# Kernel tuning notes

Hardware: AMD Instinct MI355X
Metric: run time of the kernel (lower is better)

## Reference

```python
import jax, jax.numpy as jnp
import numpy as np

B, T, D, H, O = 128, 2048, 128, 1024, 32
LAST = 20          # last_n_outputs
ALPHA = 0.9        # leak rate
SPARSITY = 0.8


def _make_w_r(rng):
    # Faithful to torch __init__: randn, /max, sparsify, /spectral radius
    w_r = rng.standard_normal((H, H))
    w_r = w_r / np.max(w_r)
    w_r = np.where(rng.random(w_r.shape) < SPARSITY, 0.0, w_r)
    max_abs_eig = np.max(np.abs(np.linalg.eigvals(w_r)))
    return (w_r / max_abs_eig).astype(np.float32)


def setup_inputs() -> dict:
    key = jax.random.key(0)
    k_x, k_in, k_w, k_b = jax.random.split(key, 4)
    rng = np.random.default_rng(0)
    x = jax.random.normal(k_x, (B, T, D), dtype=jnp.float32)
    w_in = jax.random.normal(k_in, (D, H), dtype=jnp.float32) * 0.2
    w_r = jnp.asarray(_make_w_r(rng))
    W = jax.random.normal(k_w, (H * LAST, O), dtype=jnp.float32) * 0.02
    b = jax.random.normal(k_b, (O,), dtype=jnp.float32) * 0.02
    return {"x": x, "w_in": w_in, "w_r": w_r, "W": W, "b": b}


def reference(x, w_in, w_r, W, b):
    # Precompute the non-recurrent term in one batched GEMM: [B,T,H]
    xw = jnp.einsum('btd,dh->bth', x, w_in)

    # t == 0: h0 = 0, and original code sets h = h_hat (no leaky mix)
    h = jnp.tanh(xw[:, 0])  # [B, H]

    def step(h, xt):
        h_hat = jnp.tanh(xt + h @ w_r)
        return (1.0 - ALPHA) * h + ALPHA * h_hat, None

    # steps 1 .. T-LAST-1 : no outputs collected
    xw_mid = jnp.swapaxes(xw[:, 1:T - LAST], 0, 1)   # [T-LAST-1, B, H]
    h, _ = jax.lax.scan(step, h, xw_mid)

    def step_out(h, xt):
        h_hat = jnp.tanh(xt + h @ w_r)
        h_new = (1.0 - ALPHA) * h + ALPHA * h_hat
        return h_new, h_new

    # last LAST steps: collect hidden states
    xw_tail = jnp.swapaxes(xw[:, T - LAST:], 0, 1)   # [LAST, B, H]
    _, hs = jax.lax.scan(step_out, h, xw_tail)       # [LAST, B, H]

    # concat in time order along feature dim -> [B, LAST*H]
    out_cat = jnp.transpose(hs, (1, 0, 2)).reshape(B, LAST * H)
    return out_cat @ W + b
```

## Files before the change

### kernel.cpp

```cpp
#include <hip/hip_runtime.h>
#include <stdint.h>
#include <stddef.h>

#define B_    128
#define T_    2048
#define D_    128
#define H_    1024
#define O_    32
#define LAST_ 20

#define NB_   8
#define NC_   16
#define RING_ 4

typedef __bf16 bf16x8 __attribute__((ext_vector_type(8)));
typedef __bf16 bf16x4 __attribute__((ext_vector_type(4)));
typedef float  f32x4  __attribute__((ext_vector_type(4)));

union Pack8  { unsigned long long u;    bf16x4 v; };
union Pack16 { unsigned long long u[2]; bf16x8 v; };

__device__ __forceinline__ float tanh_fast(float s) {
    float a = fminf(fmaxf(s, -12.0f), 12.0f);
    float e = __expf(2.0f * a);
    return (e - 1.0f) / (e + 1.0f);
}

__global__ __launch_bounds__(256, 1) void esn_persist(
    const float* __restrict__ x, const float* __restrict__ w_in,
    const float* __restrict__ w_r, __bf16* __restrict__ h_ex,
    float* __restrict__ hs)
{
    __shared__ bf16x8 ls[2][16][128];

    const int wg  = (int)blockIdx.x;
    const int bb  = wg & (NB_ - 1);
    const int cb  = wg >> 3;
    const int tid = (int)threadIdx.x;
    const int wv  = tid >> 6;
    const int ln  = tid & 63;
    const int nn  = ln & 15;
    const int q   = ln >> 4;
    const int b0  = bb * 16;
    const int n0  = cb * 64 + wv * 16;

    bf16x8 win[4];
    #pragma unroll
    for (int c = 0; c < 4; ++c) {
        bf16x8 f;
        #pragma unroll
        for (int j = 0; j < 8; ++j)
            f[j] = (__bf16)w_in[(size_t)(c * 32 + q * 8 + j) * H_ + (n0 + nn)];
        win[c] = f;
    }
    bf16x8 wr[32];
    #pragma unroll
    for (int kc = 0; kc < 32; ++kc) {
        bf16x8 f;
        #pragma unroll
        for (int j = 0; j < 8; ++j)
            f[j] = (__bf16)w_r[(size_t)(kc * 32 + q * 8 + j) * H_ + (n0 + nn)];
        wr[kc] = f;
    }

    const unsigned long long tdead =
        __builtin_amdgcn_s_memrealtime() + 300000000ull;

    const float* xrow = x + (size_t)(b0 + nn) * T_ * D_ + q * 8;
    const size_t hrow = (size_t)(b0 + nn) * H_;

    f32x4 xn[8];
    bf16x8 xf[4];
    {
        #pragma unroll
        for (int c = 0; c < 4; ++c) {
            xn[2 * c]     = *(const f32x4*)(xrow + c * 32);
            xn[2 * c + 1] = *(const f32x4*)(xrow + c * 32 + 4);
        }
        #pragma unroll
        for (int c = 0; c < 4; ++c) {
            bf16x8 f;
            #pragma unroll
            for (int j = 0; j < 4; ++j) {
                f[j]     = (__bf16)xn[2 * c][j];
                f[j + 4] = (__bf16)xn[2 * c + 1][j];
            }
            xf[c] = f;
        }
    }

    float hm0 = 0.f, hm1 = 0.f, hm2 = 0.f, hm3 = 0.f;

    for (int t = 0; t < T_; ++t) {
        {
            const int tn = (t + 1 < T_) ? t + 1 : T_ - 1;
            const float* xp = xrow + (size_t)tn * D_;
            #pragma unroll
            for (int c = 0; c < 4; ++c) {
                xn[2 * c]     = *(const f32x4*)(xp + c * 32);
                xn[2 * c + 1] = *(const f32x4*)(xp + c * 32 + 4);
            }
        }

        f32x4 acc0 = {0.f, 0.f, 0.f, 0.f};
        f32x4 acc1 = {0.f, 0.f, 0.f, 0.f};
        f32x4 acc2 = {0.f, 0.f, 0.f, 0.f};
        f32x4 acc3 = {0.f, 0.f, 0.f, 0.f};

        #pragma unroll
        for (int c = 0; c < 4; ++c)
            acc0 = __builtin_amdgcn_mfma_f32_16x16x32_bf16(win[c], xf[c], acc0, 0, 0, 0);

        if (t > 0) {
            const unsigned long long want =
                (unsigned long long)((((t - 1) >> 2) & 1) ^ 1);
            const int sb = (t - 1) & 1;
            const __bf16* hbase = h_ex
                + (size_t)((t - 1) & (RING_ - 1)) * (B_ * H_) + (size_t)b0 * H_;
            Pack16 pk[8];
            int spins = 0;
            for (;;) {
                #pragma unroll
                for (int i = 0; i < 8; ++i) {
                    const int p = wv * 512 + i * 64 + ln;
                    const unsigned long long* gp = (const unsigned long long*)
                        (hbase + (size_t)(p >> 7) * H_ + (p & 127) * 8);
                    pk[i].u[0] = __hip_atomic_load(gp, __ATOMIC_RELAXED,
                                                   __HIP_MEMORY_SCOPE_AGENT);
                    pk[i].u[1] = __hip_atomic_load(gp + 1, __ATOMIC_RELAXED,
                                                   __HIP_MEMORY_SCOPE_AGENT);
                }
                unsigned ok = 1u;
                #pragma unroll
                for (int i = 0; i < 8; ++i) {
                    ok &= (unsigned)((pk[i].u[0] & 1ull) == want);
                    ok &= (unsigned)((pk[i].u[1] & 1ull) == want);
                }
                if (__all(ok != 0u)) break;
                __builtin_amdgcn_s_sleep(1);
                if (((++spins) & 63) == 0 &&
                    __builtin_amdgcn_s_memrealtime() > tdead) break;
            }

            #pragma unroll
            for (int i = 0; i < 8; ++i) {
                const int p = wv * 512 + i * 64 + ln;
                const int r = p >> 7, ch = p & 127;
                ls[sb][r][ch ^ (r & 7)] = pk[i].v;
            }

            __syncthreads();

            #pragma unroll
            for (int kc = 0; kc < 32; ++kc) {
                bf16x8 a = ls[sb][nn][(kc * 4 + q) ^ (nn & 7)];
                if      ((kc & 3) == 0) acc0 = __builtin_amdgcn_mfma_f32_16x16x32_bf16(wr[kc], a, acc0, 0, 0, 0);
                else if ((kc & 3) == 1) acc1 = __builtin_amdgcn_mfma_f32_16x16x32_bf16(wr[kc], a, acc1, 0, 0, 0);
                else if ((kc & 3) == 2) acc2 = __builtin_amdgcn_mfma_f32_16x16x32_bf16(wr[kc], a, acc2, 0, 0, 0);
                else                    acc3 = __builtin_amdgcn_mfma_f32_16x16x32_bf16(wr[kc], a, acc3, 0, 0, 0);
            }
        }

        const f32x4 acc = (acc0 + acc1) + (acc2 + acc3);
        const float th0 = tanh_fast(acc[0]);
        const float th1 = tanh_fast(acc[1]);
        const float th2 = tanh_fast(acc[2]);
        const float th3 = tanh_fast(acc[3]);
        if (t == 0) {
            hm0 = th0; hm1 = th1; hm2 = th2; hm3 = th3;
        } else {
            hm0 = 0.1f * hm0 + 0.9f * th0;
            hm1 = 0.1f * hm1 + 0.9f * th1;
            hm2 = 0.1f * hm2 + 0.9f * th2;
            hm3 = 0.1f * hm3 + 0.9f * th3;
        }

        {
            Pack8 p;
            p.v = (bf16x4){(__bf16)hm0, (__bf16)hm1, (__bf16)hm2, (__bf16)hm3};
            p.u = (p.u & ~1ull) | (unsigned long long)(((t >> 2) & 1) ^ 1);
            unsigned long long* op = (unsigned long long*)
                (h_ex + (size_t)(t & (RING_ - 1)) * (B_ * H_) + hrow + n0 + q * 4);
            __hip_atomic_store(op, p.u, __ATOMIC_RELAXED,
                               __HIP_MEMORY_SCOPE_AGENT);
        }

        if (t >= T_ - LAST_) {
            f32x4* sp = (f32x4*)(hs + (size_t)(t - (T_ - LAST_)) * (B_ * H_)
                                    + hrow + n0 + q * 4);
            *sp = (f32x4){hm0, hm1, hm2, hm3};
        }
        #pragma unroll
        for (int c = 0; c < 4; ++c) {
            bf16x8 f;
            #pragma unroll
            for (int j = 0; j < 4; ++j) {
                f[j]     = (__bf16)xn[2 * c][j];
                f[j + 4] = (__bf16)xn[2 * c + 1][j];
            }
            xf[c] = f;
        }
    }
}

__global__ __launch_bounds__(256) void esn_out(
    const float* __restrict__ hs, const float* __restrict__ Wm,
    const float* __restrict__ bias, float* __restrict__ out)
{
    const int b   = (int)blockIdx.x;
    const int tid = (int)threadIdx.x;
    float acc[O_];
    #pragma unroll
    for (int o = 0; o < O_; ++o) acc[o] = 0.f;

    for (int k = tid; k < LAST_ * H_; k += 256) {
        const float hv = hs[(size_t)(k >> 10) * (B_ * H_) + (size_t)b * H_ + (k & (H_ - 1))];
        const f32x4* wp = (const f32x4*)(Wm + (size_t)k * O_);
        #pragma unroll
        for (int v = 0; v < 8; ++v) {
            f32x4 w4 = wp[v];
            acc[4 * v + 0] = fmaf(hv, w4[0], acc[4 * v + 0]);
            acc[4 * v + 1] = fmaf(hv, w4[1], acc[4 * v + 1]);
            acc[4 * v + 2] = fmaf(hv, w4[2], acc[4 * v + 2]);
            acc[4 * v + 3] = fmaf(hv, w4[3], acc[4 * v + 3]);
        }
    }

    __shared__ float red[256][O_ + 1];
    #pragma unroll
    for (int o = 0; o < O_; ++o) red[tid][o] = acc[o];
    __syncthreads();
    if (tid < O_) {
        float s = bias[tid];
        for (int i = 0; i < 256; ++i) s += red[i][tid];
        out[(size_t)b * O_ + tid] = s;
    }
}

extern "C" void kernel_launch(void* const* d_in, const int* in_sizes, int n_in,
                              void* d_out, int out_size, void* d_ws, size_t ws_size,
                              hipStream_t stream)
{
    const float* x    = (const float*)d_in[0];
    const float* w_in = (const float*)d_in[1];
    const float* w_r  = (const float*)d_in[2];
    const float* Wm   = (const float*)d_in[3];
    const float* bias = (const float*)d_in[4];
    float* out        = (float*)d_out;

    const size_t flag_bytes = 4096;
    const size_t hex_bytes  = (size_t)RING_ * B_ * H_ * sizeof(__bf16);
    const size_t hs_bytes   = (size_t)LAST_ * B_ * H_ * sizeof(float);
    if (ws_size < flag_bytes + hex_bytes + hs_bytes) return;

    __bf16* h_ex  = (__bf16*)((char*)d_ws + flag_bytes);
    float*  hs    = (float*)((char*)d_ws + flag_bytes + hex_bytes);

    hipMemsetAsync(h_ex, 0xAA, hex_bytes, stream);

    hipLaunchKernelGGL(esn_persist, dim3(NB_ * NC_), dim3(256), 0, stream,
                       x, w_in, w_r, h_ex, hs);
    hipLaunchKernelGGL(esn_out, dim3(B_), dim3(256), 0, stream,
                       hs, Wm, bias, out);
}
```

Measured before the change: 6.125 ms.

## Add XCC-local fast path for hidden-state exchange with global fallback ring

Each workgroup records its XCC id in a flag array, and the groups sharing a batch block vote on whether they all sit on the same XCC. If they do, the hidden state is also written to a second ring with sc0 stores and read back with non-temporal sc0 loads, so the exchange stays in XCC-local cache instead of going through device-scope coherence. The fast read polls with a bounded budget and gives up after two failed attempts, falling back to the original agent-scope ring. The parity tag now sits in two bits per 64-bit word, and the MFMA accumulation is split across eight accumulators instead of four. The cost is an extra store per step and a second ring in the workspace, and correctness of the fast path rests on cache-coherence behaviour that is not guaranteed.

```diff
diff --git a/kernel.cpp b/kernel.cpp
--- a/kernel.cpp
+++ b/kernel.cpp
@@ -16,9 +16,10 @@
 typedef __bf16 bf16x8 __attribute__((ext_vector_type(8)));
 typedef __bf16 bf16x4 __attribute__((ext_vector_type(4)));
 typedef float  f32x4  __attribute__((ext_vector_type(4)));
+typedef unsigned int u32x4 __attribute__((ext_vector_type(4)));
 
 union Pack8  { unsigned long long u;    bf16x4 v; };
-union Pack16 { unsigned long long u[2]; bf16x8 v; };
+union Pack16 { unsigned long long u[2]; u32x4 d; bf16x8 v; };
 
 __device__ __forceinline__ float tanh_fast(float s) {
     float a = fminf(fmaxf(s, -12.0f), 12.0f);
@@ -28,8 +29,9 @@
 
 __global__ __launch_bounds__(256, 1) void esn_persist(
     const float* __restrict__ x, const float* __restrict__ w_in,
-    const float* __restrict__ w_r, __bf16* __restrict__ h_ex,
-    float* __restrict__ hs)
+    const float* __restrict__ w_r, __bf16* __restrict__ h_exA,
+    __bf16* __restrict__ h_exB, float* __restrict__ hs,
+    int* __restrict__ flags)
 {
     __shared__ bf16x8 ls[2][16][128];
 
@@ -44,6 +46,16 @@
     const int b0  = bb * 16;
     const int n0  = cb * 64 + wv * 16;
 
+    const unsigned long long tdead =
+        __builtin_amdgcn_s_memrealtime() + 300000000ull;
+
+    int xcc;
+    asm volatile("s_getreg_b32 %0, hwreg(HW_REG_XCC_ID)" : "=s"(xcc));
+    const int mytag = 0x5A5A0000 | (xcc & 0xFF);
+    if (tid == 0)
+        __hip_atomic_store(flags + wg, mytag, __ATOMIC_RELAXED,
+                           __HIP_MEMORY_SCOPE_AGENT);
+
     bf16x8 win[4];
     #pragma unroll
     for (int c = 0; c < 4; ++c) {
@@ -63,8 +75,24 @@
         wr[kc] = f;
     }
 
-    const unsigned long long tdead =
-        __builtin_amdgcn_s_memrealtime() + 300000000ull;
+    bool votefast;
+    {
+        int alleq = 0;
+        for (;;) {
+            int seen = 1; alleq = 1;
+            #pragma unroll
+            for (int k = 0; k < NC_; ++k) {
+                int v = __hip_atomic_load(flags + (bb + 8 * k), __ATOMIC_RELAXED,
+                                          __HIP_MEMORY_SCOPE_AGENT);
+                seen  &= (int)((v & 0xFFFF0000) == 0x5A5A0000);
+                alleq &= (int)(v == mytag);
+            }
+            if (seen) break;
+            __builtin_amdgcn_s_sleep(8);
+            if (__builtin_amdgcn_s_memrealtime() > tdead) { alleq = 0; break; }
+        }
+        votefast = (alleq != 0);
+    }
 
     const float* xrow = x + (size_t)(b0 + nn) * T_ * D_ + q * 8;
     const size_t hrow = (size_t)(b0 + nn) * H_;
@@ -90,6 +118,7 @@
     }
 
     float hm0 = 0.f, hm1 = 0.f, hm2 = 0.f, hm3 = 0.f;
+    int ftrips = 0;
 
     for (int t = 0; t < T_; ++t) {
         {
@@ -102,44 +131,77 @@
             }
         }
 
-        f32x4 acc0 = {0.f, 0.f, 0.f, 0.f};
-        f32x4 acc1 = {0.f, 0.f, 0.f, 0.f};
-        f32x4 acc2 = {0.f, 0.f, 0.f, 0.f};
-        f32x4 acc3 = {0.f, 0.f, 0.f, 0.f};
+        f32x4 acc[8];
+        #pragma unroll
+        for (int i = 0; i < 8; ++i) acc[i] = (f32x4){0.f, 0.f, 0.f, 0.f};
 
         #pragma unroll
         for (int c = 0; c < 4; ++c)
-            acc0 = __builtin_amdgcn_mfma_f32_16x16x32_bf16(win[c], xf[c], acc0, 0, 0, 0);
+            acc[c] = __builtin_amdgcn_mfma_f32_16x16x32_bf16(win[c], xf[c], acc[c], 0, 0, 0);
 
         if (t > 0) {
-            const unsigned long long want =
-                (unsigned long long)((((t - 1) >> 2) & 1) ^ 1);
+            const unsigned long long want1 =
+                (unsigned long long)((((t - 1) >> 2) & 1) ^ 1) * 0x100000001ull;
             const int sb = (t - 1) & 1;
-            const __bf16* hbase = h_ex
-                + (size_t)((t - 1) & (RING_ - 1)) * (B_ * H_) + (size_t)b0 * H_;
+            const size_t slotoff =
+                (size_t)((t - 1) & (RING_ - 1)) * (B_ * H_) + (size_t)b0 * H_;
             Pack16 pk[8];
-            int spins = 0;
-            for (;;) {
-                #pragma unroll
-                for (int i = 0; i < 8; ++i) {
-                    const int p = wv * 512 + i * 64 + ln;
-                    const unsigned long long* gp = (const unsigned long long*)
-                        (hbase + (size_t)(p >> 7) * H_ + (p & 127) * 8);
-                    pk[i].u[0] = __hip_atomic_load(gp, __ATOMIC_RELAXED,
-                                                   __HIP_MEMORY_SCOPE_AGENT);
-                    pk[i].u[1] = __hip_atomic_load(gp + 1, __ATOMIC_RELAXED,
-                                                   __HIP_MEMORY_SCOPE_AGENT);
+            bool have = false;
+
+            if (votefast && ftrips < 2) {
+                const __bf16* hbase = h_exA + slotoff;
+                int budget = (t == 1) ? 768 : 160;
+                for (;;) {
+                    #pragma unroll
+                    for (int i = 0; i < 8; ++i) {
+                        const int p = wv * 512 + i * 64 + ln;
+                        const __bf16* gp = hbase + (size_t)(p >> 7) * H_ + (p & 127) * 8;
+                        asm volatile("global_load_dwordx4 %0, %1, off sc0 nt"
+                                     : "=v"(pk[i].d) : "v"(gp) : "memory");
+                    }
+                    asm volatile("s_waitcnt vmcnt(0)"
+                                 : "+v"(pk[0].d), "+v"(pk[1].d), "+v"(pk[2].d),
+                                   "+v"(pk[3].d), "+v"(pk[4].d), "+v"(pk[5].d),
+                                   "+v"(pk[6].d), "+v"(pk[7].d) :: "memory");
+                    __builtin_amdgcn_sched_barrier(0);
+                    unsigned ok = 1u;
+                    #pragma unroll
+                    for (int i = 0; i < 8; ++i) {
+                        ok &= (unsigned)(((pk[i].u[0] ^ want1) & 0x100000001ull) == 0);
+                        ok &= (unsigned)(((pk[i].u[1] ^ want1) & 0x100000001ull) == 0);
+                    }
+                    if (__all(ok != 0u)) { have = true; break; }
+                    __builtin_amdgcn_s_sleep(1);
+                    if (--budget == 0) break;
                 }
-                unsigned ok = 1u;
-                #pragma unroll
-                for (int i = 0; i < 8; ++i) {
-                    ok &= (unsigned)((pk[i].u[0] & 1ull) == want);
-                    ok &= (unsigned)((pk[i].u[1] & 1ull) == want);
+                if (!have) ++ftrips;
+            }
+
+            if (!have) {
+                const __bf16* hbase = h_exB + slotoff;
+                int spins = 0;
+                for (;;) {
+                    #pragma unroll
+                    for (int i = 0; i < 8; ++i) {
+                        const int p = wv * 512 + i * 64 + ln;
+                        const unsigned long long* gp = (const unsigned long long*)
+                            (hbase + (size_t)(p >> 7) * H_ + (p & 127) * 8);
+                        pk[i].u[0] = __hip_atomic_load(gp, __ATOMIC_RELAXED,
+                                                       __HIP_MEMORY_SCOPE_AGENT);
+                        pk[i].u[1] = __hip_atomic_load(gp + 1, __ATOMIC_RELAXED,
+                                                       __HIP_MEMORY_SCOPE_AGENT);
+                    }
+                    unsigned ok = 1u;
+                    #pragma unroll
+                    for (int i = 0; i < 8; ++i) {
+                        ok &= (unsigned)(((pk[i].u[0] ^ want1) & 0x100000001ull) == 0);
+                        ok &= (unsigned)(((pk[i].u[1] ^ want1) & 0x100000001ull) == 0);
+                    }
+                    if (__all(ok != 0u)) break;
+                    __builtin_amdgcn_s_sleep(1);
+                    if (((++spins) & 63) == 0 &&
+                        __builtin_amdgcn_s_memrealtime() > tdead) break;
                 }
-                if (__all(ok != 0u)) break;
-                __builtin_amdgcn_s_sleep(1);
-                if (((++spins) & 63) == 0 &&
-                    __builtin_amdgcn_s_memrealtime() > tdead) break;
             }
 
             #pragma unroll
@@ -154,18 +216,16 @@
             #pragma unroll
             for (int kc = 0; kc < 32; ++kc) {
                 bf16x8 a = ls[sb][nn][(kc * 4 + q) ^ (nn & 7)];
-                if      ((kc & 3) == 0) acc0 = __builtin_amdgcn_mfma_f32_16x16x32_bf16(wr[kc], a, acc0, 0, 0, 0);
-                else if ((kc & 3) == 1) acc1 = __builtin_amdgcn_mfma_f32_16x16x32_bf16(wr[kc], a, acc1, 0, 0, 0);
-                else if ((kc & 3) == 2) acc2 = __builtin_amdgcn_mfma_f32_16x16x32_bf16(wr[kc], a, acc2, 0, 0, 0);
-                else                    acc3 = __builtin_amdgcn_mfma_f32_16x16x32_bf16(wr[kc], a, acc3, 0, 0, 0);
-            }
-        }
-
-        const f32x4 acc = (acc0 + acc1) + (acc2 + acc3);
-        const float th0 = tanh_fast(acc[0]);
-        const float th1 = tanh_fast(acc[1]);
-        const float th2 = tanh_fast(acc[2]);
-        const float th3 = tanh_fast(acc[3]);
+                acc[kc & 7] = __builtin_amdgcn_mfma_f32_16x16x32_bf16(wr[kc], a, acc[kc & 7], 0, 0, 0);
+            }
+        }
+
+        const f32x4 asum = ((acc[0] + acc[4]) + (acc[1] + acc[5]))
+                         + ((acc[2] + acc[6]) + (acc[3] + acc[7]));
+        const float th0 = tanh_fast(asum[0]);
+        const float th1 = tanh_fast(asum[1]);
+        const float th2 = tanh_fast(asum[2]);
+        const float th3 = tanh_fast(asum[3]);
         if (t == 0) {
             hm0 = th0; hm1 = th1; hm2 = th2; hm3 = th3;
         } else {
@@ -178,10 +238,18 @@
         {
             Pack8 p;
             p.v = (bf16x4){(__bf16)hm0, (__bf16)hm1, (__bf16)hm2, (__bf16)hm3};
-            p.u = (p.u & ~1ull) | (unsigned long long)(((t >> 2) & 1) ^ 1);
-            unsigned long long* op = (unsigned long long*)
-                (h_ex + (size_t)(t & (RING_ - 1)) * (B_ * H_) + hrow + n0 + q * 4);
-            __hip_atomic_store(op, p.u, __ATOMIC_RELAXED,
+            const unsigned long long tg =
+                (unsigned long long)(((t >> 2) & 1) ^ 1) * 0x100000001ull;
+            p.u = (p.u & ~0x100000001ull) | tg;
+            const size_t poff = (size_t)(t & (RING_ - 1)) * (B_ * H_)
+                                + hrow + n0 + q * 4;
+            if (votefast) {
+                unsigned long long* opA = (unsigned long long*)(h_exA + poff);
+                asm volatile("global_store_dwordx2 %0, %1, off sc0"
+                             :: "v"(opA), "v"(p.u) : "memory");
+            }
+            unsigned long long* opB = (unsigned long long*)(h_exB + poff);
+            __hip_atomic_store(opB, p.u, __ATOMIC_RELAXED,
                                __HIP_MEMORY_SCOPE_AGENT);
         }
 
@@ -249,17 +317,20 @@
     float* out        = (float*)d_out;
 
     const size_t flag_bytes = 4096;
-    const size_t hex_bytes  = (size_t)RING_ * B_ * H_ * sizeof(__bf16);
+    const size_t ring_bytes = (size_t)RING_ * B_ * H_ * sizeof(__bf16);
     const size_t hs_bytes   = (size_t)LAST_ * B_ * H_ * sizeof(float);
-    if (ws_size < flag_bytes + hex_bytes + hs_bytes) return;
-
-    __bf16* h_ex  = (__bf16*)((char*)d_ws + flag_bytes);
-    float*  hs    = (float*)((char*)d_ws + flag_bytes + hex_bytes);
-
-    hipMemsetAsync(h_ex, 0xAA, hex_bytes, stream);
+    if (ws_size < flag_bytes + 2 * ring_bytes + hs_bytes) return;
+
+    int*    flags = (int*)d_ws;
+    __bf16* h_exA = (__bf16*)((char*)d_ws + flag_bytes);
+    __bf16* h_exB = (__bf16*)((char*)d_ws + flag_bytes + ring_bytes);
+    float*  hs    = (float*)((char*)d_ws + flag_bytes + 2 * ring_bytes);
+
+    hipMemsetAsync(flags, 0x00, flag_bytes, stream);
+    hipMemsetAsync(h_exA, 0xAA, 2 * ring_bytes, stream);
 
     hipLaunchKernelGGL(esn_persist, dim3(NB_ * NC_), dim3(256), 0, stream,
-                       x, w_in, w_r, h_ex, hs);
+                       x, w_in, w_r, h_exA, h_exB, hs, flags);
     hipLaunchKernelGGL(esn_out, dim3(B_), dim3(256), 0, stream,
                        hs, Wm, bias, out);
 }
```

New measurement: 7.024 ms. +14.7%, slower.
